# Kernel tuning notes

Hardware: AMD Instinct MI355X
Metric: run time of the kernel (lower is better)

The kernel has to match this reference:

```python
import jax, jax.numpy as jnp
import numpy as np

EPS = 1e-8
MIN_VAL = -1e7  # module default min_val=-10000000.0


def _div_safe(n, d):
    return n / jnp.maximum(d, EPS)


def _cosine_pairwise(v1, v2):
    # v1: (B,L1,H), v2: (B,L2,H) -> (B,L1,L2)
    n1 = jnp.linalg.norm(v1, axis=2, keepdims=True)
    n2 = jnp.linalg.norm(v2, axis=2, keepdims=True)
    a = jnp.einsum('bik,bjk->bij', v1, v2)
    return _div_safe(a, n1 * jnp.swapaxes(n2, 1, 2))


def _masked_max(v, mask, axis, keepdims=False):
    rep = jnp.where(mask > 0, v, MIN_VAL)
    val = jnp.max(rep, axis=axis, keepdims=keepdims)
    m = jnp.max(jnp.broadcast_to(mask, v.shape), axis=axis, keepdims=keepdims)
    return val * m


def _masked_mean(v, mask, axis, keepdims=False):
    s = jnp.sum(v * mask, axis=axis, keepdims=keepdims)
    c = jnp.sum(jnp.broadcast_to(mask, v.shape), axis=axis, keepdims=keepdims)
    return _div_safe(s, c)


def _cos_sim(a, b, axis):
    # torch F.cosine_similarity semantics: dot / (max(|a|,eps)*max(|b|,eps))
    dot = jnp.sum(a * b, axis=axis)
    na = jnp.maximum(jnp.linalg.norm(a, axis=axis), EPS)
    nb = jnp.maximum(jnp.linalg.norm(b, axis=axis), EPS)
    return dot / (na * nb)


def _mpm(v1, v2, w):
    # v1, v2: (B,L,H); w: (P,H) -> ((B,L,1), (B,L,P))
    mv1 = _cos_sim(v1, v2, 2)[..., None]
    v1w = w[None, None] * v1[:, :, None, :]  # (B,L,P,H)
    v2w = w[None, None] * v2[:, :, None, :]
    return mv1, _cos_sim(v1w, v2w, 3)


def _mpm_pairwise(v1, v2, w):
    # v1: (B,L1,H), v2: (B,L2,H), w: (P,H) -> (B,L1,L2,P)
    v1w = w[None, :, None, :] * v1[:, None, :, :]  # (B,P,L1,H)
    v2w = w[None, :, None, :] * v2[:, None, :, :]  # (B,P,L2,H)
    n1 = jnp.linalg.norm(v1w, axis=3, keepdims=True)
    n2 = jnp.linalg.norm(v2w, axis=3, keepdims=True)
    n = jnp.einsum('bpik,bpjk->bpij', v1w, v2w)
    d = n1 * jnp.swapaxes(n2, 2, 3)
    return jnp.transpose(_div_safe(n, d), (0, 2, 3, 1))


def setup_inputs() -> dict:
    key = jax.random.key(0)
    ks = jax.random.split(key, 8)
    B, L, H, P = 32, 128, 100, 20
    return {
        'context_p': jax.random.normal(ks[0], (B, L, H), dtype=jnp.float32),
        'mask_p': jax.random.randint(ks[1], (B, L), 0, 2, dtype=jnp.int32),
        'context_h': jax.random.normal(ks[2], (B, L, H), dtype=jnp.float32),
        'mask_h': jax.random.randint(ks[3], (B, L), 0, 2, dtype=jnp.int32),
        'w0': jax.random.uniform(ks[4], (P, H), dtype=jnp.float32),
        'w1': jax.random.uniform(ks[5], (P, H), dtype=jnp.float32),
        'w2': jax.random.uniform(ks[6], (P, H), dtype=jnp.float32),
        'w3': jax.random.uniform(ks[7], (P, H), dtype=jnp.float32),
    }


def reference(context_p, mask_p, context_h, mask_h, w0, w1, w2, w3):
    mask_p = mask_p.astype(jnp.float32)
    mask_h = mask_h.astype(jnp.float32)
    B, Lp, H = context_p.shape
    Lh = context_h.shape[1]

    mask_p_h = mask_p[:, :, None] * mask_h[:, None, :]   # (B,Lp,Lh)
    mask_h_p = jnp.swapaxes(mask_p_h, 1, 2)              # (B,Lh,Lp)
    cp = context_p * mask_p[..., None]
    ch = context_h * mask_h[..., None]

    # --- pairwise cosine + masked max/mean pooling ---
    cos = _cosine_pairwise(cp, ch)                        # (B,Lp,Lh)
    cosT = jnp.swapaxes(cos, 1, 2)
    cos_max_p = _masked_max(cos, mask_p_h, 2, True)
    cos_mean_p = _masked_mean(cos, mask_p_h, 2, True)
    cos_max_h = _masked_max(cosT, mask_h_p, 2, True)
    cos_mean_h = _masked_mean(cosT, mask_h_p, 2, True)

    # --- full match (is_forward=True: last real token) ---
    idx_p = jnp.clip(jnp.sum(mask_p, 1).astype(jnp.int32) - 1, 0)[:, None, None]
    idx_h = jnp.clip(jnp.sum(mask_h, 1).astype(jnp.int32) - 1, 0)[:, None, None]
    cp_last = jnp.take_along_axis(cp, jnp.broadcast_to(idx_p, (B, 1, H)), axis=1)
    ch_last = jnp.take_along_axis(ch, jnp.broadcast_to(idx_h, (B, 1, H)), axis=1)
    mv_p_f1, mv_p_fP = _mpm(cp, jnp.broadcast_to(ch_last, (B, Lp, H)), w0)
    mv_h_f1, mv_h_fP = _mpm(ch, jnp.broadcast_to(cp_last, (B, Lh, H)), w0)

    # --- maxpool match ---
    mv_max = _mpm_pairwise(cp, ch, w1)                    # (B,Lp,Lh,P)
    mv_p_max = _masked_max(mv_max, mask_p_h[..., None], 2)
    mv_p_mean = _masked_mean(mv_max, mask_p_h[..., None], 2)
    mv_maxT = jnp.transpose(mv_max, (0, 2, 1, 3))
    mv_h_max = _masked_max(mv_maxT, mask_h_p[..., None], 2)
    mv_h_mean = _masked_mean(mv_maxT, mask_h_p[..., None], 2)

    # --- attentive match (mean) ---
    att_mean_h = _div_safe(jnp.einsum('bij,bjh->bih', cos, ch),
                           jnp.sum(cos, 2, keepdims=True))
    att_mean_p = _div_safe(jnp.einsum('bij,bih->bjh', cos, cp),
                           jnp.swapaxes(jnp.sum(cos, 1, keepdims=True), 1, 2))
    mv_p_am1, mv_p_amP = _mpm(cp, att_mean_h, w2)
    mv_h_am1, mv_h_amP = _mpm(ch, att_mean_p, w2)

    # --- max-attentive match ---
    att_h = ch[:, None, :, :] * cos[:, :, :, None]        # (B,Lp,Lh,H)
    att_p_t = cp[:, None, :, :] * cosT[:, :, :, None]     # (B,Lh,Lp,H) == att_p.permute(0,2,1,3)
    att_max_h = _masked_max(att_h, mask_p_h[..., None], 2)
    att_max_p = _masked_max(att_p_t, mask_h_p[..., None], 2)
    mv_p_ax1, mv_p_axP = _mpm(cp, att_max_h, w3)
    mv_h_ax1, mv_h_axP = _mpm(ch, att_max_p, w3)

    mv_p = jnp.concatenate([cos_max_p, cos_mean_p, mv_p_f1, mv_p_fP,
                            mv_p_max, mv_p_mean, mv_p_am1, mv_p_amP,
                            mv_p_ax1, mv_p_axP], axis=2)
    mv_h = jnp.concatenate([cos_max_h, cos_mean_h, mv_h_f1, mv_h_fP,
                            mv_h_max, mv_h_mean, mv_h_am1, mv_h_amP,
                            mv_h_ax1, mv_h_axP], axis=2)
    return mv_p, mv_h
```

## Files before the change

### kernel.cpp

```cpp
#include <hip/hip_runtime.h>
#include <math.h>


namespace {
constexpr int B = 32;
constexpr int L = 128;
constexpr int H = 100;
constexpr int P = 20;
constexpr int C = 105;
constexpr int TI = 8;
constexpr int SMEM_BYTES = 40768;
constexpr float EPSF = 1e-8f;
constexpr float MINV = -1e7f;
}

typedef unsigned short u16;
typedef unsigned int u32;
typedef short sh8 __attribute__((ext_vector_type(8)));
typedef float f4 __attribute__((ext_vector_type(4)));

__device__ __forceinline__ u16 f2bf(float f) {
    u32 u = __float_as_uint(f);
    u += 0x7FFFu + ((u >> 16) & 1u);
    return (u16)(u >> 16);
}
__device__ __forceinline__ float bf2f(u32 h) {
    return __uint_as_float(h << 16);
}
__device__ __forceinline__ u32 pack2(float a, float b) {
    return (u32)f2bf(a) | ((u32)f2bf(b) << 16);
}
__device__ __forceinline__ sh8 zfrag() {
    return __builtin_bit_cast(sh8, (uint4){0u, 0u, 0u, 0u});
}

__global__ __launch_bounds__(512) void
k_prep(const float* __restrict__ ctx_p, const int* __restrict__ mask_p,
       const float* __restrict__ ctx_h, const int* __restrict__ mask_h,
       const float* __restrict__ w1,
       float* __restrict__ cp, float* __restrict__ ch,
       u16* __restrict__ cpb, u16* __restrict__ chb,
       float* __restrict__ np_, float* __restrict__ nh_,
       float* __restrict__ nwp, float* __restrict__ nwh)
{
    const int bx = blockIdx.x, b = blockIdx.y, side = blockIdx.z, t = threadIdx.x;
    const int i0 = bx * 8;
    const float* ctx = side ? ctx_h : ctx_p;
    const int*  mask = side ? mask_h : mask_p;
    float* dst  = side ? ch  : cp;
    u16*   dstb = side ? chb : cpb;
    float* nrm  = side ? nh_ : np_;
    float* nw   = side ? nwh : nwp;

    __shared__ __align__(16) float sv2[8][112];

    #pragma unroll
    for (int it = 0; it < 2; ++it) {
        int idx = it * 512 + t;
        int rr = idx >> 7, k = idx & 127;
        const int row = b * L + i0 + rr;
        const float m = (float)mask[row];
        float v = 0.f;
        if (k < H) {
            v = ctx[(size_t)row * H + k] * m;
            dst[(size_t)row * H + k] = v;
            sv2[rr][k] = v * v;
        }
        dstb[(size_t)row * 128 + k] = f2bf(v);
    }
    __syncthreads();

    const int wv = t >> 6, ln = t & 63;
    if (ln < 63) {
        const int g = ln / 3, seg = ln - 3 * g;
        const int k0 = (seg == 0) ? 0 : (seg == 1) ? 8 : 16;
        const int k1 = (seg == 0) ? 8 : (seg == 1) ? 16 : 25;
        const float4* v4 = (const float4*)sv2[wv];
        float acc = 0.f;
        if (g < P) {
            const float4* w4 = (const float4*)(w1 + g * H);
            for (int k = k0; k < k1; ++k) {
                float4 w = w4[k], s = v4[k];
                acc += w.x * w.x * s.x + w.y * w.y * s.y +
                       w.z * w.z * s.z + w.w * w.w * s.w;
            }
        } else {
            for (int k = k0; k < k1; ++k) {
                float4 s = v4[k];
                acc += s.x + s.y + s.z + s.w;
            }
        }
        float a1 = __shfl(acc, ln + 1), a2 = __shfl(acc, ln + 2);
        if (seg == 0) {
            const int row = b * L + i0 + wv;
            float s = sqrtf(acc + a1 + a2);
            if (g < P) nw[(size_t)row * P + g] = s;
            else       nrm[row] = s;
        }
    }
}

__global__ __launch_bounds__(512) void
k_main(const float* __restrict__ cp, const float* __restrict__ ch,
       const u16* __restrict__ cpb, const u16* __restrict__ chb,
       const float* __restrict__ np_, const float* __restrict__ nh_,
       const float* __restrict__ nw1p, const float* __restrict__ nw1h,
       const int* __restrict__ mask_p, const int* __restrict__ mask_h,
       const float* __restrict__ w0, const float* __restrict__ w1,
       const float* __restrict__ w2, const float* __restrict__ w3,
       float* __restrict__ out)
{
    __shared__ __align__(16) char smem[SMEM_BYTES];
    const int bx = blockIdx.x, b = blockIdx.y, t = threadIdx.x;
    const int wv = t >> 6, ln = t & 63;
    float* out_p = out;
    float* out_h = out + (size_t)B * L * C;

    if (bx < P) {
        const int p = bx;
        u16*  sB    = (u16*)smem;
        float* snwA = (float*)(smem + 26624);
        float* snwB = (float*)(smem + 27136);
        float* smA  = (float*)(smem + 27648);
        float* smB  = (float*)(smem + 28160);
        float* pJmax= (float*)(smem + 28672);
        float* pJsum= (float*)(smem + 29184);
        float* pImax= (float*)(smem + 29696);
        float* pIsum= (float*)(smem + 33792);
        float* sRed = (float*)(smem + 37888);

        if (t < 128) {
            snwA[t] = nw1p[(b * L + t) * P + p];
            snwB[t] = nw1h[(b * L + t) * P + p];
            smA[t] = (float)mask_p[b * L + t];
            smB[t] = (float)mask_h[b * L + t];
        }
        __syncthreads();

        if (t < 64) {
            float a0 = smB[t], a1 = smB[t + 64];
            float mx = fmaxf(a0, a1), sm = a0 + a1;
            for (int d = 1; d < 64; d <<= 1) {
                mx = fmaxf(mx, __shfl_xor(mx, d));
                sm += __shfl_xor(sm, d);
            }
            if (t == 0) { sRed[2] = mx; sRed[3] = sm; }
        } else if (t < 128) {
            const int l = t - 64;
            float a0 = smA[l], a1 = smA[l + 64];
            float mx = fmaxf(a0, a1), sm = a0 + a1;
            for (int d = 1; d < 64; d <<= 1) {
                mx = fmaxf(mx, __shfl_xor(mx, d));
                sm += __shfl_xor(sm, d);
            }
            if (l == 0) { sRed[0] = mx; sRed[1] = sm; }
        }

        {
            const uint4* src = (const uint4*)(chb + (size_t)b * L * 128);
            for (int idx = t; idx < 128 * 13; idx += 512) {
                int row = idx / 13, cc = idx - row * 13;
                uint4 v = src[row * 16 + cc];
                *(uint4*)&sB[row * 104 + cc * 8] = v;
            }
        }
        __syncthreads();

        const int m = ln & 15, q = ln >> 4;

        float swv[4][8];
        #pragma unroll
        for (int ks = 0; ks < 4; ++ks)
            #pragma unroll
            for (int e = 0; e < 8; ++e) {
                int k = ks * 32 + q * 8 + e;
                float w = (k < H) ? w1[p * H + k] : 0.f;
                swv[ks][e] = w * w;
            }

        f4 acc[8];
        #pragma unroll
        for (int ct = 0; ct < 8; ++ct) acc[ct] = (f4){0.f, 0.f, 0.f, 0.f};

        const uint4* gA = (const uint4*)(cpb + (size_t)(b * L + wv * 16 + m) * 128);

        #pragma unroll
        for (int ks = 0; ks < 4; ++ks) {
            uint4 va = gA[ks * 4 + q];
            sh8 af;
            {
                u32 vs[4] = {va.x, va.y, va.z, va.w};
                u32 r[4];
                #pragma unroll
                for (int e = 0; e < 4; ++e) {
                    float f0 = bf2f(vs[e] & 0xffffu) * swv[ks][2 * e];
                    float f1 = bf2f(vs[e] >> 16) * swv[ks][2 * e + 1];
                    r[e] = (u32)f2bf(f0) | ((u32)f2bf(f1) << 16);
                }
                uint4 o = {r[0], r[1], r[2], r[3]};
                af = __builtin_bit_cast(sh8, o);
            }
            const int ko = ks * 32 + q * 8;
            const bool oob = (ks == 3) && (q > 0);
            #pragma unroll
            for (int ct = 0; ct < 8; ++ct) {
                sh8 bb = oob ? zfrag() : *(const sh8*)&sB[(ct * 16 + m) * 104 + ko];
                acc[ct] = __builtin_amdgcn_mfma_f32_16x16x32_bf16(af, bb, acc[ct], 0, 0, 0);
            }
        }

        float nB[8], mBv[8], imax[8], isum[8];
        #pragma unroll
        for (int ct = 0; ct < 8; ++ct) {
            const int j = ct * 16 + m;
            nB[ct] = snwB[j]; mBv[ct] = smB[j];
            imax[ct] = MINV; isum[ct] = 0.f;
        }
        #pragma unroll
        for (int reg = 0; reg < 4; ++reg) {
            const int i = wv * 16 + q * 4 + reg;
            const float na = snwA[i];
            const float ma = smA[i];
            float jmax = MINV, jsum = 0.f;
            #pragma unroll
            for (int ct = 0; ct < 8; ++ct) {
                float v = acc[ct][reg] *
                          __builtin_amdgcn_rcpf(fmaxf(na * nB[ct], EPSF));
                jmax = fmaxf(jmax, mBv[ct] > 0.f ? v : MINV);
                jsum += mBv[ct] > 0.f ? v : 0.f;
                imax[ct] = fmaxf(imax[ct], ma > 0.f ? v : MINV);
                isum[ct] += ma > 0.f ? v : 0.f;
            }
            for (int d = 1; d < 16; d <<= 1) {
                jmax = fmaxf(jmax, __shfl_xor(jmax, d));
                jsum += __shfl_xor(jsum, d);
            }
            if (m == 0) { pJmax[i] = jmax; pJsum[i] = jsum; }
        }
        #pragma unroll
        for (int ct = 0; ct < 8; ++ct) {
            float mx = imax[ct], sm = isum[ct];
            mx = fmaxf(mx, __shfl_xor(mx, 16)); sm += __shfl_xor(sm, 16);
            mx = fmaxf(mx, __shfl_xor(mx, 32)); sm += __shfl_xor(sm, 32);
            if (q == 0) { const int j = ct * 16 + m; pImax[wv * 128 + j] = mx; pIsum[wv * 128 + j] = sm; }
        }
        __syncthreads();

        if (t < 128) {
            const int i = t;
            const float ma = smA[i];
            const float mm = ma * sRed[2];
            const float cnt = ma * sRed[3];
            float* orow = out_p + ((size_t)b * L + i) * C;
            orow[23 + p] = pJmax[i] * mm;
            orow[43 + p] = ma * pJsum[i] / fmaxf(cnt, EPSF);

            const float mb = smB[i];
            float hmax = MINV, hsum = 0.f;
            #pragma unroll
            for (int s = 0; s < 8; ++s) {
                hmax = fmaxf(hmax, pImax[s * 128 + i]);
                hsum += pIsum[s * 128 + i];
            }
            float* hrow = out_h + ((size_t)b * L + i) * C;
            hrow[23 + p] = hmax * mb * sRed[0];
            hrow[43 + p] = mb * hsum / fmaxf(mb * sRed[1], EPSF);
        }
    } else {
        const int e = bx - P;
        const int side = e >> 4, tile = e & 15;
        const int i0 = tile * TI;
        const float* Bv  = side ? cp : ch;
        const float* A   = side ? ch : cp;
        const u16*  Ab16 = side ? chb : cpb;
        const u16*  Bvb  = side ? cpb : chb;
        const float* nA_ = side ? nh_ : np_;
        const float* nB_ = side ? np_ : nh_;
        const int* maskA = side ? mask_h : mask_p;
        const int* maskB = side ? mask_p : mask_h;
        float* outBase = out + ((size_t)side * B * L + (size_t)b * L) * C;

        float* scosC = (float*)(smem + 26624);
        float* sa    = (float*)(smem + 30720);
        float* sam   = (float*)(smem + 33920);
        float* sax   = (float*)(smem + 37120);
        float* sl    = (float*)(smem + 40320);
        float* snB   = (float*)(smem + 33920);
        float* snA   = (float*)(smem + 34432);
        u16*  cidx  = (u16*)(smem + 34464);
        int*   pnv   = (int*)(smem + 40720);

        scosC[t] = 0.f;
        scosC[t + 512] = 0.f;
        if (wv == 0) {
            int m0 = maskB[b * L + ln], m1 = maskB[b * L + 64 + ln];
            unsigned long long b0 = __ballot(m0 > 0);
            unsigned long long b1 = __ballot(m1 > 0);
            unsigned long long pre = (1ull << ln) - 1ull;
            int n0 = __popcll(b0);
            if (m0 > 0) cidx[__popcll(b0 & pre)] = (u16)ln;
            if (m1 > 0) cidx[n0 + __popcll(b1 & pre)] = (u16)(64 + ln);
            if (ln == 0) *pnv = n0 + __popcll(b1);
        } else if (wv >= 2) {
            for (int x = t - 128; x < TI * 128; x += 384) {
                int il = x >> 7, k = x & 127;
                if (k < H) sa[il * 100 + k] = A[((size_t)b * L + i0 + il) * H + k];
            }
        }
        __syncthreads();
        const int nv = *pnv;
        const int nct = (nv + 15) >> 4;

        {
            const uint4* src = (const uint4*)(Bvb + (size_t)b * L * 128);
            for (int c = t; c < nct * 208; c += 512) {
                int jj = c / 13, cc = c - jj * 13;
                uint4 v;
                if (jj < nv) v = src[(int)cidx[jj] * 16 + cc];
                else { v.x = v.y = v.z = v.w = 0u; }
                *(uint4*)(smem + jj * 208 + cc * 16) = v;
            }
            if (t < 128) snB[t] = (t < nv) ? nB_[b * L + (int)cidx[t]] : 0.f;
            else if (t < 136) snA[t - 128] = nA_[b * L + i0 + (t - 128)];
            if (wv == 1) {
                int last = nv - 1; if (last < 0) last = 0;
                const float* lr = Bv + ((size_t)b * L + last) * H;
                sl[ln] = lr[ln];
                if (ln + 64 < H) sl[ln + 64] = lr[ln + 64];
            }
        }
        __syncthreads();

        const int m = ln & 15, q = ln >> 4;
        if (wv < nct) {
            const uint4* gA = (const uint4*)(Ab16 + (size_t)(b * L + i0 + (m & 7)) * 128);
            f4 acc0 = (f4){0.f, 0.f, 0.f, 0.f};
            #pragma unroll
            for (int ks = 0; ks < 4; ++ks) {
                uint4 va = gA[ks * 4 + q];
                if (m >= 8) { va.x = va.y = va.z = va.w = 0u; }
                sh8 af = __builtin_bit_cast(sh8, va);
                const int ko2 = (ks * 32 + q * 8) * 2;
                const bool oob = (ks == 3) && (q > 0);
                sh8 bb = oob ? zfrag()
                             : *(const sh8*)(smem + (wv * 16 + m) * 208 + ko2);
                acc0 = __builtin_amdgcn_mfma_f32_16x16x32_bf16(af, bb, acc0, 0, 0, 0);
            }
            if (q < 2) {
                #pragma unroll
                for (int reg = 0; reg < 4; ++reg) {
                    const int i = q * 4 + reg;
                    const int jj = wv * 16 + m;
                    scosC[i * 128 + jj] = acc0[reg] *
                        __builtin_amdgcn_rcpf(fmaxf(snA[i] * snB[jj], EPSF));
                }
            }
        }
        __syncthreads();

        {
            const int il = wv;
            const int gi = i0 + il;
            const float mA = (float)maskA[b * L + gi];
            float c0 = scosC[il * 128 + ln], c1 = scosC[il * 128 + 64 + ln];
            float scj = c0 + c1;
            float mv0 = (ln < nv) ? c0 : MINV;
            float mv1 = (ln + 64 < nv) ? c1 : MINV;
            float cmx = fmaxf(mv0, mv1);
            for (int d = 1; d < 64; d <<= 1) {
                scj += __shfl_xor(scj, d);
                cmx = fmaxf(cmx, __shfl_xor(cmx, d));
            }
            const float mm = (nv > 0) ? mA : 0.f;
            if (ln == 0) {
                float* orow = outBase + (size_t)gi * C;
                orow[0] = cmx * mm;
                orow[1] = mA * scj / fmaxf(mA * (float)nv, EPSF);
            }
            if (ln < 50) {
                float am0 = 0.f, am1 = 0.f, ax0 = MINV, ax1 = MINV;
                const u32* bp = (const u32*)smem + ln;
                const float* cr = scosC + il * 128;
                #pragma unroll 4
                for (int jj = 0; jj < nv; ++jj) {
                    u32 pk = bp[jj * 52];
                    float cj = cr[jj];
                    float v0 = cj * __uint_as_float(pk << 16);
                    float v1 = cj * __uint_as_float(pk & 0xffff0000u);
                    am0 += v0; am1 += v1;
                    ax0 = fmaxf(ax0, v0); ax1 = fmaxf(ax1, v1);
                }
                const float rs = __builtin_amdgcn_rcpf(fmaxf(scj, EPSF));
                sam[il * 100 + 2 * ln] = am0 * rs; sam[il * 100 + 2 * ln + 1] = am1 * rs;
                sax[il * 100 + 2 * ln] = ax0 * mm; sax[il * 100 + 2 * ln + 1] = ax1 * mm;
            }
        }
        __syncthreads();

        for (int idx = t; idx < 64 * 13; idx += 512) {
            int row = idx / 13, cc = idx - row * 13;
            int kc = cc * 8;
            int il = row >> 3, col = row & 7;
            const float* sa_il  = sa  + il * 100;
            const float* sam_il = sam + il * 100;
            const float* sax_il = sax + il * 100;
            const float* p1 = (col >= 4) ? (col == 4 ? sl : col == 5 ? sam_il : sax_il)
                                         : sa_il;
            const float* p2 = (col == 0 || col == 4) ? sl :
                              (col == 1 || col == 5) ? sam_il :
                              (col == 2 || col == 6) ? sax_il : sa_il;
            u32 ow[4];
            #pragma unroll
            for (int e2 = 0; e2 < 4; ++e2) {
                int k0 = kc + 2 * e2;
                float f0 = (col < 7 && k0 < H)     ? p1[k0] * p2[k0]         : 0.f;
                float f1 = (col < 7 && k0 + 1 < H) ? p1[k0 + 1] * p2[k0 + 1] : 0.f;
                ow[e2] = pack2(f0, f1);
            }
            uint4 o = {ow[0], ow[1], ow[2], ow[3]};
            *(uint4*)(smem + row * 208 + kc * 2) = o;
        }
        for (int idx = t; idx < 64 * 13; idx += 512) {
            int kc = (idx % 13) * 8;
            int row = idx / 13;
            u32 ow[4];
            #pragma unroll
            for (int e2 = 0; e2 < 4; ++e2) {
                int k0 = kc + 2 * e2;
                float f0 = 0.f, f1 = 0.f;
                if (row < 60) {
                    const float* wr = (row < 20) ? w0 + row * H :
                                      (row < 40) ? w2 + (row - 20) * H :
                                                   w3 + (row - 40) * H;
                    if (k0 < H)     { float w = wr[k0];     f0 = w * w; }
                    if (k0 + 1 < H) { float w = wr[k0 + 1]; f1 = w * w; }
                } else if (row == 60) {
                    f0 = (k0 < H) ? 1.f : 0.f;
                    f1 = (k0 + 1 < H) ? 1.f : 0.f;
                }
                ow[e2] = pack2(f0, f1);
            }
            uint4 o = {ow[0], ow[1], ow[2], ow[3]};
            *(uint4*)(smem + 13312 + row * 208 + kc * 2) = o;
        }
        __syncthreads();

        f4 d3[4];
        #pragma unroll
        for (int Mt = 0; Mt < 4; ++Mt) d3[Mt] = (f4){0.f, 0.f, 0.f, 0.f};
        {
            const int cn = m & 7;
            #pragma unroll
            for (int ks = 0; ks < 4; ++ks) {
                const int ko2 = (ks * 32 + q * 8) * 2;
                const bool oob = (ks == 3) && (q > 0);
                sh8 bb = oob ? zfrag()
                             : *(const sh8*)(smem + (wv * 8 + cn) * 208 + ko2);
                #pragma unroll
                for (int Mt = 0; Mt < 4; ++Mt) {
                    sh8 aa = oob ? zfrag()
                                 : *(const sh8*)(smem + 13312 + (Mt * 16 + m) * 208 + ko2);
                    d3[Mt] = __builtin_amdgcn_mfma_f32_16x16x32_bf16(aa, bb, d3[Mt], 0, 0, 0);
                }
            }
        }
        __syncthreads();

        if (m < 8) {
            #pragma unroll
            for (int Mt = 0; Mt < 4; ++Mt)
                #pragma unroll
                for (int reg = 0; reg < 4; ++reg)
                    ((float*)smem)[wv * 576 + (Mt * 16 + q * 4 + reg) * 9 + m] = d3[Mt][reg];
        }
        __syncthreads();

        for (int task = t; task < TI * 63; task += 512) {
            const int il = task / 63, c = task - il * 63;
            int row, dcol, nbcol, chn;
            if (c < 60) {
                const int grp = c / 20;
                row = c; dcol = grp; nbcol = 4 + grp;
                chn = ((grp == 0) ? 3 : (grp == 1) ? 64 : 85) + (c - grp * 20);
            } else {
                const int cc = c - 60;
                row = 60; dcol = cc; nbcol = 4 + cc;
                chn = (cc == 0) ? 2 : (cc == 1) ? 63 : 84;
            }
            const float* Dr = (const float*)smem + il * 576 + row * 9;
            float d = Dr[dcol], na = Dr[3], nb = Dr[nbcol];
            outBase[(size_t)(i0 + il) * C + chn] =
                d / (fmaxf(sqrtf(na), EPSF) * fmaxf(sqrtf(nb), EPSF));
        }
    }
}

extern "C" void kernel_launch(void* const* d_in, const int* in_sizes, int n_in,
                              void* d_out, int out_size, void* d_ws, size_t ws_size,
                              hipStream_t stream)
{
    const float* ctx_p = (const float*)d_in[0];
    const int*   mask_p = (const int*)d_in[1];
    const float* ctx_h = (const float*)d_in[2];
    const int*   mask_h = (const int*)d_in[3];
    const float* w0 = (const float*)d_in[4];
    const float* w1 = (const float*)d_in[5];
    const float* w2 = (const float*)d_in[6];
    const float* w3 = (const float*)d_in[7];
    float* out = (float*)d_out;

    float* ws   = (float*)d_ws;
    float* cp   = ws;
    float* ch   = cp   + B * L * H;
    float* np_  = ch   + B * L * H;
    float* nh_  = np_  + B * L;
    float* nw1p = nh_  + B * L;
    float* nw1h = nw1p + B * L * P;
    u16*   cpb  = (u16*)(nw1h + B * L * P);
    u16*   chb  = cpb + B * L * 128;

    k_prep<<<dim3(L / 8, B, 2), dim3(512), 0, stream>>>(
        ctx_p, mask_p, ctx_h, mask_h, w1,
        cp, ch, cpb, chb, np_, nh_, nw1p, nw1h);
    k_main<<<dim3(P + 32, B), dim3(512), 0, stream>>>(
        cp, ch, cpb, chb, np_, nh_, nw1p, nw1h, mask_p, mask_h,
        w0, w1, w2, w3, out);
}
```

Baseline: 124.0 us.

## Interleave row pairs in shared memory, read cosine via readlane, precompute reciprocal norms

The first kernel now precomputes reciprocal norms per row and column and multiplies them, replacing a reciprocal per element; clamping each norm at 1e-4 changes the epsilon semantics slightly. The attentive stage stores compacted B rows interleaved in pairs so each lane reads two rows with one 64-bit LDS load. The cosine row is broadcast by readlane from registers instead of LDS, and the loop is unrolled by two. The cosine MFMA now reads B fragments directly from global memory via the compacted index, removing the dependence on the LDS row layout. Entries beyond nv are masked to zero.

Measured after the change: 126.7 us. 2.2% more time.

```diff
diff --git a/kernel.cpp b/kernel.cpp
--- a/kernel.cpp
+++ b/kernel.cpp
@@ -32,6 +32,9 @@
 }
 __device__ __forceinline__ sh8 zfrag() {
     return __builtin_bit_cast(sh8, (uint4){0u, 0u, 0u, 0u});
+}
+__device__ __forceinline__ float rdlane(float v, int l) {
+    return __uint_as_float((u32)__builtin_amdgcn_readlane((int)__float_as_uint(v), l));
 }
 
 __global__ __launch_bounds__(512) void
@@ -209,23 +212,23 @@
             }
         }
 
-        float nB[8], mBv[8], imax[8], isum[8];
+        float rnB[8], mBv[8], imax[8], isum[8];
         #pragma unroll
         for (int ct = 0; ct < 8; ++ct) {
             const int j = ct * 16 + m;
-            nB[ct] = snwB[j]; mBv[ct] = smB[j];
+            rnB[ct] = __builtin_amdgcn_rcpf(fmaxf(snwB[j], 1e-4f));
+            mBv[ct] = smB[j];
             imax[ct] = MINV; isum[ct] = 0.f;
         }
         #pragma unroll
         for (int reg = 0; reg < 4; ++reg) {
             const int i = wv * 16 + q * 4 + reg;
-            const float na = snwA[i];
+            const float rna = __builtin_amdgcn_rcpf(fmaxf(snwA[i], 1e-4f));
             const float ma = smA[i];
             float jmax = MINV, jsum = 0.f;
             #pragma unroll
             for (int ct = 0; ct < 8; ++ct) {
-                float v = acc[ct][reg] *
-                          __builtin_amdgcn_rcpf(fmaxf(na * nB[ct], EPSF));
+                float v = acc[ct][reg] * (rna * rnB[ct]);
                 jmax = fmaxf(jmax, mBv[ct] > 0.f ? v : MINV);
                 jsum += mBv[ct] > 0.f ? v : 0.f;
                 imax[ct] = fmaxf(imax[ct], ma > 0.f ? v : MINV);
@@ -293,6 +296,8 @@
         scosC[t] = 0.f;
         scosC[t + 512] = 0.f;
         if (wv == 0) {
+            cidx[ln] = 0;
+            cidx[64 + ln] = 0;
             int m0 = maskB[b * L + ln], m1 = maskB[b * L + 64 + ln];
             unsigned long long b0 = __ballot(m0 > 0);
             unsigned long long b1 = __ballot(m1 > 0);
@@ -313,12 +318,18 @@
 
         {
             const uint4* src = (const uint4*)(Bvb + (size_t)b * L * 128);
-            for (int c = t; c < nct * 208; c += 512) {
-                int jj = c / 13, cc = c - jj * 13;
-                uint4 v;
-                if (jj < nv) v = src[(int)cidx[jj] * 16 + cc];
-                else { v.x = v.y = v.z = v.w = 0u; }
-                *(uint4*)(smem + jj * 208 + cc * 16) = v;
+            const int npair = (nv + 1) >> 1;
+            for (int c = t; c < npair * 13; c += 512) {
+                int p2 = c / 13, cc = c - p2 * 13;
+                uint4 v0 = src[(int)cidx[2 * p2] * 16 + cc];
+                uint4 v1;
+                if (2 * p2 + 1 < nv) v1 = src[(int)cidx[2 * p2 + 1] * 16 + cc];
+                else { v1.x = v1.y = v1.z = v1.w = 0u; }
+                u32* dst = (u32*)smem + p2 * 104 + cc * 8;
+                ((uint2*)dst)[0] = make_uint2(v0.x, v1.x);
+                ((uint2*)dst)[1] = make_uint2(v0.y, v1.y);
+                ((uint2*)dst)[2] = make_uint2(v0.z, v1.z);
+                ((uint2*)dst)[3] = make_uint2(v0.w, v1.w);
             }
             if (t < 128) snB[t] = (t < nv) ? nB_[b * L + (int)cidx[t]] : 0.f;
             else if (t < 136) snA[t - 128] = nA_[b * L + i0 + (t - 128)];
@@ -334,25 +345,25 @@
         const int m = ln & 15, q = ln >> 4;
         if (wv < nct) {
             const uint4* gA = (const uint4*)(Ab16 + (size_t)(b * L + i0 + (m & 7)) * 128);
+            const int jj = wv * 16 + m;
+            const int brow = (int)cidx[jj];
+            const uint4* gB = (const uint4*)(Bvb + (size_t)(b * L + brow) * 128);
             f4 acc0 = (f4){0.f, 0.f, 0.f, 0.f};
             #pragma unroll
             for (int ks = 0; ks < 4; ++ks) {
                 uint4 va = gA[ks * 4 + q];
                 if (m >= 8) { va.x = va.y = va.z = va.w = 0u; }
                 sh8 af = __builtin_bit_cast(sh8, va);
-                const int ko2 = (ks * 32 + q * 8) * 2;
-                const bool oob = (ks == 3) && (q > 0);
-                sh8 bb = oob ? zfrag()
-                             : *(const sh8*)(smem + (wv * 16 + m) * 208 + ko2);
+                sh8 bb = __builtin_bit_cast(sh8, gB[ks * 4 + q]);
                 acc0 = __builtin_amdgcn_mfma_f32_16x16x32_bf16(af, bb, acc0, 0, 0, 0);
             }
             if (q < 2) {
                 #pragma unroll
                 for (int reg = 0; reg < 4; ++reg) {
                     const int i = q * 4 + reg;
-                    const int jj = wv * 16 + m;
-                    scosC[i * 128 + jj] = acc0[reg] *
+                    float val = acc0[reg] *
                         __builtin_amdgcn_rcpf(fmaxf(snA[i] * snB[jj], EPSF));
+                    scosC[i * 128 + jj] = (jj < nv) ? val : 0.f;
                 }
             }
         }
@@ -379,16 +390,50 @@
             }
             if (ln < 50) {
                 float am0 = 0.f, am1 = 0.f, ax0 = MINV, ax1 = MINV;
-                const u32* bp = (const u32*)smem + ln;
-                const float* cr = scosC + il * 128;
-                #pragma unroll 4
-                for (int jj = 0; jj < nv; ++jj) {
-                    u32 pk = bp[jj * 52];
-                    float cj = cr[jj];
-                    float v0 = cj * __uint_as_float(pk << 16);
-                    float v1 = cj * __uint_as_float(pk & 0xffff0000u);
+                const u32* bp = (const u32*)smem + 2 * ln;
+                const int n0 = nv < 64 ? nv : 64;
+                int jj = 0;
+                #pragma unroll 2
+                for (; jj + 1 < n0; jj += 2) {
+                    uint2 pk = *(const uint2*)(bp + (jj >> 1) * 104);
+                    float ca = rdlane(c0, jj), cb = rdlane(c0, jj + 1);
+                    float v0a = ca * __uint_as_float(pk.x << 16);
+                    float v1a = ca * __uint_as_float(pk.x & 0xffff0000u);
+                    float v0b = cb * __uint_as_float(pk.y << 16);
+                    float v1b = cb * __uint_as_float(pk.y & 0xffff0000u);
+                    am0 += v0a + v0b; am1 += v1a + v1b;
+                    ax0 = fmaxf(fmaxf(ax0, v0a), v0b);
+                    ax1 = fmaxf(fmaxf(ax1, v1a), v1b);
+                }
+                if (jj < n0) {
+                    u32 pk = bp[(jj >> 1) * 104];
+                    float ca = rdlane(c0, jj);
+                    float v0 = ca * __uint_as_float(pk << 16);
+                    float v1 = ca * __uint_as_float(pk & 0xffff0000u);
                     am0 += v0; am1 += v1;
                     ax0 = fmaxf(ax0, v0); ax1 = fmaxf(ax1, v1);
+                }
+                if (nv > 64) {
+                    #pragma unroll 2
+                    for (jj = 64; jj + 1 < nv; jj += 2) {
+                        uint2 pk = *(const uint2*)(bp + (jj >> 1) * 104);
+                        float ca = rdlane(c1, jj - 64), cb = rdlane(c1, jj - 63);
+                        float v0a = ca * __uint_as_float(pk.x << 16);
+                        float v1a = ca * __uint_as_float(pk.x & 0xffff0000u);
+                        float v0b = cb * __uint_as_float(pk.y << 16);
+                        float v1b = cb * __uint_as_float(pk.y & 0xffff0000u);
+                        am0 += v0a + v0b; am1 += v1a + v1b;
+                        ax0 = fmaxf(fmaxf(ax0, v0a), v0b);
+                        ax1 = fmaxf(fmaxf(ax1, v1a), v1b);
+                    }
+                    if (jj < nv) {
+                        u32 pk = bp[(jj >> 1) * 104];
+                        float ca = rdlane(c1, jj - 64);
+                        float v0 = ca * __uint_as_float(pk << 16);
+                        float v1 = ca * __uint_as_float(pk & 0xffff0000u);
+                        am0 += v0; am1 += v1;
+                        ax0 = fmaxf(ax0, v0); ax1 = fmaxf(ax1, v1);
+                    }
                 }
                 const float rs = __builtin_amdgcn_rcpf(fmaxf(scj, EPSF));
                 sam[il * 100 + 2 * ln] = am0 * rs; sam[il * 100 + 2 * ln + 1] = am1 * rs;
```
